# Kernel optimization log

Measured on AMD Instinct MI355X. Metric: run time of the kernel, lower is better.

## Reference

```python
import jax, jax.numpy as jnp
import numpy as np

WINDOW_SIZE = 11
SIGMA = 1.5
C1 = 0.01 ** 2
C2 = 0.03 ** 2


def _gaussian_window(window_size, sigma, channel, dtype=jnp.float32):
    x = np.arange(window_size) - window_size // 2
    g = np.exp(-(x.astype(np.float64) ** 2) / (2.0 * sigma ** 2))
    g = (g / g.sum()).astype(np.float32)
    w2d = np.outer(g, g)  # [K, K]
    # depthwise kernel: [C, 1, K, K] (OIHW with feature_group_count=C)
    w = np.broadcast_to(w2d, (channel, 1, window_size, window_size))
    return jnp.asarray(w, dtype=dtype)


def _dw_conv(x, window):
    # x: [B, C, H, W]; window: [C, 1, K, K]; SAME padding via pad=K//2 (K odd)
    k = window.shape[-1]
    p = k // 2
    return jax.lax.conv_general_dilated(
        x, window,
        window_strides=(1, 1),
        padding=((p, p), (p, p)),
        dimension_numbers=("NCHW", "OIHW", "NCHW"),
        feature_group_count=x.shape[1],
    )


def setup_inputs() -> dict:
    key = jax.random.key(0)
    k1, k2 = jax.random.split(key)
    shape = (32, 3, 512, 512)
    img1 = jax.random.uniform(k1, shape, dtype=jnp.float32)
    img2 = jax.random.uniform(k2, shape, dtype=jnp.float32)
    return {"img1": img1, "img2": img2}


def reference(img1, img2):
    channel = img1.shape[1]
    window = _gaussian_window(WINDOW_SIZE, SIGMA, channel, img1.dtype)

    mu1 = _dw_conv(img1, window)
    mu2 = _dw_conv(img2, window)
    mu1_sq = mu1 * mu1
    mu2_sq = mu2 * mu2
    mu1_mu2 = mu1 * mu2

    sigma1_sq = _dw_conv(img1 * img1, window) - mu1_sq
    sigma2_sq = _dw_conv(img2 * img2, window) - mu2_sq
    sigma12 = _dw_conv(img1 * img2, window) - mu1_mu2

    ssim_map = ((2.0 * mu1_mu2 + C1) * (2.0 * sigma12 + C2)) / (
        (mu1_sq + mu2_sq + C1) * (sigma1_sq + sigma2_sq + C2)
    )
    return 1.0 - jnp.mean(ssim_map)
```

## Files before the change

### kernel.cpp

```cpp
#include <hip/hip_runtime.h>

#define HH 512
#define WW 512
#define PLANES 96
#define RSTRIP 32
#define NPIX 25165824.0f

#define G0 0.2660117f
#define G1 0.2130056f
#define G2 0.1093607f
#define G3 0.0360008f
#define G4 0.0075988f
#define G5 0.0010284f

#define C1F 1e-4f
#define C2F 9e-4f

typedef float v2f __attribute__((ext_vector_type(2)));
#define PKFMA(a, b, c) __builtin_elementwise_fma(a, b, c)

#define DECL_HIST2(Z) v2f Z##0={0,0},Z##1={0,0},Z##2={0,0},Z##3={0,0},Z##4={0,0},\
                          Z##5={0,0},Z##6={0,0},Z##7={0,0},Z##8={0,0},Z##9={0,0},Z##10={0,0}
#define SHIFT_HIST(Z) do{Z##0=Z##1;Z##1=Z##2;Z##2=Z##3;Z##3=Z##4;Z##4=Z##5;\
                         Z##5=Z##6;Z##6=Z##7;Z##7=Z##8;Z##8=Z##9;Z##9=Z##10;}while(0)
#define VCONV2(Z) PKFMA(g5, Z##0+Z##10, PKFMA(g4, Z##1+Z##9, PKFMA(g3, Z##2+Z##8,\
                  PKFMA(g2, Z##3+Z##7, PKFMA(g1, Z##4+Z##6, g0*Z##5)))))

#define HCONV(T0,T1,T2,T3,T4,T5,T6,T7,T8,T9,T10, NAB, NPQ) do { \
    NAB = g0 * (T5);            NPQ = g0 * ((T5) * (T5)); \
    NAB = PKFMA(g1, (T4)+(T6),  NAB); NPQ = PKFMA(g1, PKFMA((T4),(T4),(T6)*(T6)),   NPQ); \
    NAB = PKFMA(g2, (T3)+(T7),  NAB); NPQ = PKFMA(g2, PKFMA((T3),(T3),(T7)*(T7)),   NPQ); \
    NAB = PKFMA(g3, (T2)+(T8),  NAB); NPQ = PKFMA(g3, PKFMA((T2),(T2),(T8)*(T8)),   NPQ); \
    NAB = PKFMA(g4, (T1)+(T9),  NAB); NPQ = PKFMA(g4, PKFMA((T1),(T1),(T9)*(T9)),   NPQ); \
    NAB = PKFMA(g5, (T0)+(T10), NAB); NPQ = PKFMA(g5, PKFMA((T0),(T0),(T10)*(T10)), NPQ); \
} while (0)

#define EPILOG(ZAB, ZPQ) do { \
    const v2f mu = VCONV2(ZAB); \
    const v2f c2 = VCONV2(ZPQ); \
    const float a = mu.x * mu.x; \
    const float b = mu.y * mu.y; \
    const float musq = 0.5f  * (a + b);        \
    const float mu12 = 0.25f * (a - b);        \
    const float csq  = 0.5f  * (c2.x + c2.y);  \
    const float cxy  = 0.25f * (c2.x - c2.y);  \
    const float ssum = csq - musq; \
    const float s12  = cxy - mu12; \
    const float num = fmaf(2.f, mu12, C1F) * fmaf(2.f, s12, C2F); \
    const float den = (musq + C1F) * (ssum + C2F); \
    lsum += num * __builtin_amdgcn_rcpf(den); \
} while (0)

__global__ __launch_bounds__(256) __attribute__((amdgpu_waves_per_eu(3, 8)))
void ssim_main(const float* __restrict__ img1,
               const float* __restrict__ img2,
               float* __restrict__ acc) {
    __shared__ __align__(16) v2f luv[4][144];
    const int tid  = threadIdx.x;
    const int lane = tid & 63;
    const int wv   = tid >> 6;
    const int base = wv * 128;
    const int r0   = blockIdx.y * RSTRIP;
    const int p    = blockIdx.z;
    const size_t pb = (size_t)p * (HH * WW);
    const int c0   = base + 2 * lane;

    const bool hl = (lane < 5);
    const bool hhalo = (lane < 12);
    int hcol = hl ? (base - 5 + lane) : (base + 123 + lane);
    const bool hv = hhalo && ((unsigned)hcol < (unsigned)WW);
    if (!hv) hcol = 0;
    const int hslot = hl ? lane : (128 + lane);

    const float* rx = img1 + pb + (ptrdiff_t)(r0 - 5) * WW + c0;
    const float* ry = img2 + pb + (ptrdiff_t)(r0 - 5) * WW + c0;
    const float* hx = img1 + pb + (ptrdiff_t)(r0 - 5) * WW + hcol;
    const float* hy = img2 + pb + (ptrdiff_t)(r0 - 5) * WW + hcol;

    const v2f g0 = {G0, G0}, g1 = {G1, G1}, g2 = {G2, G2},
              g3 = {G3, G3}, g4 = {G4, G4}, g5 = {G5, G5};

    DECL_HIST2(ABe); DECL_HIST2(PQe);
    DECL_HIST2(ABo); DECL_HIST2(PQo);

    v2f cxv = {0.f, 0.f}, cyv = {0.f, 0.f};
    float chx = 0.f, chy = 0.f;
    if ((unsigned)(r0 - 5) < (unsigned)HH) {
        __builtin_memcpy(&cxv, rx, 8);
        __builtin_memcpy(&cyv, ry, 8);
        if (hv) { chx = hx[0]; chy = hy[0]; }
    }

    v2f* const sb = &luv[wv][0];
    float lsum = 0.f;
    const int tend = r0 + RSTRIP + 4;

#pragma unroll 6
    for (int t = r0 - 5; t <= tend; ++t, rx += WW, ry += WW, hx += WW, hy += WW) {
        SHIFT_HIST(ABe); SHIFT_HIST(PQe); SHIFT_HIST(ABo); SHIFT_HIST(PQo);

        v2f nxv = {0.f, 0.f}, nyv = {0.f, 0.f};
        float nhx = 0.f, nhy = 0.f;
        const int tn = t + 1;
        if (tn <= tend && (unsigned)tn < (unsigned)HH) {
            __builtin_memcpy(&nxv, rx + WW, 8);
            __builtin_memcpy(&nyv, ry + WW, 8);
            if (hv) { nhx = hx[WW]; nhy = hy[WW]; }
        }

        v2f nABe = {0,0}, nPQe = {0,0}, nABo = {0,0}, nPQo = {0,0};
        if ((unsigned)t < (unsigned)HH) {
            const v2f u2 = cxv + cyv;
            const v2f w2 = cxv - cyv;
            sb[2 * lane + 5] = v2f{u2.x, w2.x};
            sb[2 * lane + 6] = v2f{u2.y, w2.y};
            if (hhalo) sb[hslot] = v2f{chx + chy, chx - chy};
            __asm__ volatile("" ::: "memory");
            __builtin_amdgcn_wave_barrier();

            const v2f* wp = sb + 2 * lane;
            const v2f t0 = wp[0], t1 = wp[1], t2 = wp[2],  t3 = wp[3];
            const v2f t4 = wp[4], t5 = wp[5], t6 = wp[6],  t7 = wp[7];
            const v2f t8 = wp[8], t9 = wp[9], ta = wp[10], tb = wp[11];
            HCONV(t0,t1,t2,t3,t4,t5,t6,t7,t8,t9,ta, nABe, nPQe);
            HCONV(t1,t2,t3,t4,t5,t6,t7,t8,t9,ta,tb, nABo, nPQo);
            __asm__ volatile("" ::: "memory");
            __builtin_amdgcn_wave_barrier();
        }
        cxv = nxv; cyv = nyv; chx = nhx; chy = nhy;
        ABe10 = nABe; PQe10 = nPQe; ABo10 = nABo; PQo10 = nPQo;

        const int s = t - 5 - r0;
        if ((unsigned)s < (unsigned)RSTRIP) {
            EPILOG(ABe, PQe);
            EPILOG(ABo, PQo);
        }
    }

#pragma unroll
    for (int off = 32; off > 0; off >>= 1)
        lsum += __shfl_down(lsum, off, 64);
    __shared__ float ws4[4];
    if (lane == 0) ws4[wv] = lsum;
    __syncthreads();
    if (threadIdx.x == 0)
        atomicAdd(acc, ws4[0] + ws4[1] + ws4[2] + ws4[3]);
}

__global__ void ssim_zero(float* acc) { acc[0] = 0.f; }

__global__ void ssim_finalize(const float* __restrict__ acc, float* __restrict__ out) {
    out[0] = 1.f - acc[0] * (1.f / NPIX);
}

extern "C" void kernel_launch(void* const* d_in, const int* in_sizes, int n_in,
                              void* d_out, int out_size, void* d_ws, size_t ws_size,
                              hipStream_t stream) {
    const float* img1 = (const float*)d_in[0];
    const float* img2 = (const float*)d_in[1];
    float* out = (float*)d_out;
    float* acc = (float*)d_ws;

    ssim_zero<<<1, 1, 0, stream>>>(acc);
    dim3 grid(1, HH / RSTRIP, PLANES);
    ssim_main<<<grid, 256, 0, stream>>>(img1, img2, acc);
    ssim_finalize<<<1, 1, 0, stream>>>(acc, out);
}
```

Before: 257.2 us.

## Double-buffer per-wave LDS row to overlap loads with horizontal conv

Splits the per-wave shared-memory row buffer into two alternating slots. Each iteration reads the current row from LDS and runs the horizontal convolution while the next row's global loads are issued and then written into the other slot. This removes the wave barriers, the compiler memory fences and the per-row validity branch around the convolution; rows outside the image are written as zeros instead. It also raises the minimum waves-per-EU hint from 3 to 4 and addresses the halo column as an offset from the main pointer. The cost is twice the LDS per block and tighter register limits, which could cause spills.

Measured after the change: 364.6 us. 1.42x slower.

```diff
diff --git a/kernel.cpp b/kernel.cpp
--- a/kernel.cpp
+++ b/kernel.cpp
@@ -51,11 +51,11 @@
     lsum += num * __builtin_amdgcn_rcpf(den); \
 } while (0)
 
-__global__ __launch_bounds__(256) __attribute__((amdgpu_waves_per_eu(3, 8)))
+__global__ __launch_bounds__(256) __attribute__((amdgpu_waves_per_eu(4, 8)))
 void ssim_main(const float* __restrict__ img1,
                const float* __restrict__ img2,
                float* __restrict__ acc) {
-    __shared__ __align__(16) v2f luv[4][144];
+    __shared__ __align__(16) v2f luv[2][4][144];
     const int tid  = threadIdx.x;
     const int lane = tid & 63;
     const int wv   = tid >> 6;
@@ -69,13 +69,12 @@
     const bool hhalo = (lane < 12);
     int hcol = hl ? (base - 5 + lane) : (base + 123 + lane);
     const bool hv = hhalo && ((unsigned)hcol < (unsigned)WW);
-    if (!hv) hcol = 0;
-    const int hslot = hl ? lane : (128 + lane);
+    if (!hv) hcol = c0;
+    const int hdelta = hcol - c0;
+    const int hslot  = hl ? lane : (128 + lane);
 
     const float* rx = img1 + pb + (ptrdiff_t)(r0 - 5) * WW + c0;
     const float* ry = img2 + pb + (ptrdiff_t)(r0 - 5) * WW + c0;
-    const float* hx = img1 + pb + (ptrdiff_t)(r0 - 5) * WW + hcol;
-    const float* hy = img2 + pb + (ptrdiff_t)(r0 - 5) * WW + hcol;
 
     const v2f g0 = {G0, G0}, g1 = {G1, G1}, g2 = {G2, G2},
               g3 = {G3, G3}, g4 = {G4, G4}, g5 = {G5, G5};
@@ -83,51 +82,54 @@
     DECL_HIST2(ABe); DECL_HIST2(PQe);
     DECL_HIST2(ABo); DECL_HIST2(PQo);
 
-    v2f cxv = {0.f, 0.f}, cyv = {0.f, 0.f};
-    float chx = 0.f, chy = 0.f;
-    if ((unsigned)(r0 - 5) < (unsigned)HH) {
-        __builtin_memcpy(&cxv, rx, 8);
-        __builtin_memcpy(&cyv, ry, 8);
-        if (hv) { chx = hx[0]; chy = hy[0]; }
+    {
+        const int t0 = r0 - 5;
+        v2f xa = {0.f, 0.f}, yb = {0.f, 0.f};
+        float hx0 = 0.f, hy0 = 0.f;
+        if ((unsigned)t0 < (unsigned)HH) {
+            __builtin_memcpy(&xa, rx, 8);
+            __builtin_memcpy(&yb, ry, 8);
+            if (hv) { hx0 = rx[hdelta]; hy0 = ry[hdelta]; }
+        }
+        v2f* sb = &luv[t0 & 1][wv][0];
+        const v2f u2 = xa + yb, w2 = xa - yb;
+        sb[2 * lane + 5] = v2f{u2.x, w2.x};
+        sb[2 * lane + 6] = v2f{u2.y, w2.y};
+        if (hhalo) sb[hslot] = v2f{hx0 + hy0, hx0 - hy0};
     }
 
-    v2f* const sb = &luv[wv][0];
     float lsum = 0.f;
     const int tend = r0 + RSTRIP + 4;
 
 #pragma unroll 6
-    for (int t = r0 - 5; t <= tend; ++t, rx += WW, ry += WW, hx += WW, hy += WW) {
+    for (int t = r0 - 5; t <= tend; ++t, rx += WW, ry += WW) {
         SHIFT_HIST(ABe); SHIFT_HIST(PQe); SHIFT_HIST(ABo); SHIFT_HIST(PQo);
 
-        v2f nxv = {0.f, 0.f}, nyv = {0.f, 0.f};
-        float nhx = 0.f, nhy = 0.f;
-        const int tn = t + 1;
-        if (tn <= tend && (unsigned)tn < (unsigned)HH) {
-            __builtin_memcpy(&nxv, rx + WW, 8);
-            __builtin_memcpy(&nyv, ry + WW, 8);
-            if (hv) { nhx = hx[WW]; nhy = hy[WW]; }
+        const v2f* wp = &luv[t & 1][wv][0] + 2 * lane;
+        const v2f t0 = wp[0], t1 = wp[1], t2 = wp[2],  t3 = wp[3];
+        const v2f t4 = wp[4], t5 = wp[5], t6 = wp[6],  t7 = wp[7];
+        const v2f t8 = wp[8], t9 = wp[9], ta = wp[10], tb = wp[11];
+
+        v2f xa = {0.f, 0.f}, yb = {0.f, 0.f};
+        float hx0 = 0.f, hy0 = 0.f;
+        if ((unsigned)(t + 1) < (unsigned)HH) {
+            __builtin_memcpy(&xa, rx + WW, 8);
+            __builtin_memcpy(&yb, ry + WW, 8);
+            if (hv) { hx0 = rx[WW + hdelta]; hy0 = ry[WW + hdelta]; }
         }
 
         v2f nABe = {0,0}, nPQe = {0,0}, nABo = {0,0}, nPQo = {0,0};
-        if ((unsigned)t < (unsigned)HH) {
-            const v2f u2 = cxv + cyv;
-            const v2f w2 = cxv - cyv;
+        HCONV(t0,t1,t2,t3,t4,t5,t6,t7,t8,t9,ta, nABe, nPQe);
+        HCONV(t1,t2,t3,t4,t5,t6,t7,t8,t9,ta,tb, nABo, nPQo);
+
+        {
+            v2f* sb = &luv[(t + 1) & 1][wv][0];
+            const v2f u2 = xa + yb, w2 = xa - yb;
             sb[2 * lane + 5] = v2f{u2.x, w2.x};
             sb[2 * lane + 6] = v2f{u2.y, w2.y};
-            if (hhalo) sb[hslot] = v2f{chx + chy, chx - chy};
-            __asm__ volatile("" ::: "memory");
-            __builtin_amdgcn_wave_barrier();
+            if (hhalo) sb[hslot] = v2f{hx0 + hy0, hx0 - hy0};
+        }
 
-            const v2f* wp = sb + 2 * lane;
-            const v2f t0 = wp[0], t1 = wp[1], t2 = wp[2],  t3 = wp[3];
-            const v2f t4 = wp[4], t5 = wp[5], t6 = wp[6],  t7 = wp[7];
-            const v2f t8 = wp[8], t9 = wp[9], ta = wp[10], tb = wp[11];
-            HCONV(t0,t1,t2,t3,t4,t5,t6,t7,t8,t9,ta, nABe, nPQe);
-            HCONV(t1,t2,t3,t4,t5,t6,t7,t8,t9,ta,tb, nABo, nPQo);
-            __asm__ volatile("" ::: "memory");
-            __builtin_amdgcn_wave_barrier();
-        }
-        cxv = nxv; cyv = nyv; chx = nhx; chy = nhy;
         ABe10 = nABe; PQe10 = nPQe; ABo10 = nABo; PQo10 = nPQo;
 
         const int s = t - 5 - r0;
```
